# Performance work log

Hardware: AMD Instinct MI355X
Metric: run time of the kernel (lower is better)

The kernel has to match this reference:

```python
import jax, jax.numpy as jnp
import numpy as np

DIM = 64
HALF = DIM // 2
K = 8
B = 3.0
HID = 256
N = 65536
MIN_BW = 1e-3
MIN_BH = 1e-3
MIN_D = 1e-3


def _mlp(x, w0, b0, w1, b1, w2, b2):
    h = jnp.tanh(x @ w0 + b0)
    h = jnp.tanh(h @ w1 + b1)
    return h @ w2 + b2


def _unconstrained_rqs(x, uW, uH, uD, tail_bound):
    # x: [N, d]; uW, uH: [N, d, K]; uD: [N, d, K-1]
    # Faithful to Durkan/Karpathy unconstrained_RQS (forward, inverse=False).
    left, right, bottom, top = -tail_bound, tail_bound, -tail_bound, tail_bound
    inside = (x >= -tail_bound) & (x <= tail_bound)

    const = float(np.log(np.exp(1.0 - MIN_D) - 1.0))
    uD = jnp.pad(uD, ((0, 0), (0, 0), (1, 1)), constant_values=const)  # [N,d,K+1]

    widths = jax.nn.softmax(uW, axis=-1)
    widths = MIN_BW + (1.0 - MIN_BW * K) * widths
    cumw = jnp.cumsum(widths, axis=-1)
    cumw = jnp.pad(cumw, ((0, 0), (0, 0), (1, 0)))
    cumw = (right - left) * cumw + left
    cumw = cumw.at[..., 0].set(left).at[..., -1].set(right)
    widths = cumw[..., 1:] - cumw[..., :-1]

    derivs = MIN_D + jax.nn.softplus(uD)  # [N,d,K+1]

    heights = jax.nn.softmax(uH, axis=-1)
    heights = MIN_BH + (1.0 - MIN_BH * K) * heights
    cumh = jnp.cumsum(heights, axis=-1)
    cumh = jnp.pad(cumh, ((0, 0), (0, 0), (1, 0)))
    cumh = (top - bottom) * cumh + bottom
    cumh = cumh.at[..., 0].set(bottom).at[..., -1].set(top)
    heights = cumh[..., 1:] - cumh[..., :-1]

    # searchsorted: sum(x >= bin_locations) - 1, with eps on the last edge
    xin = jnp.clip(x, left, right)  # safe values for the outside-interval lanes
    locs = cumw.at[..., -1].add(1e-6)
    bin_idx = jnp.sum(xin[..., None] >= locs, axis=-1) - 1
    bin_idx = jnp.clip(bin_idx, 0, K - 1)

    def g(a):
        return jnp.take_along_axis(a, bin_idx[..., None], axis=-1)[..., 0]

    in_cumw = g(cumw)
    in_w = g(widths)
    in_cumh = g(cumh)
    in_h = g(heights)
    in_delta = g(heights / widths)
    in_d = g(derivs)
    in_d1 = g(derivs[..., 1:])

    theta = (xin - in_cumw) / in_w
    tt = theta * (1.0 - theta)
    numer = in_h * (in_delta * theta * theta + in_d * tt)
    denom = in_delta + (in_d + in_d1 - 2.0 * in_delta) * tt
    out = in_cumh + numer / denom
    dnum = in_delta * in_delta * (in_d1 * theta * theta + 2.0 * in_delta * tt + in_d * (1.0 - theta) ** 2)
    lad = jnp.log(dnum) - 2.0 * jnp.log(denom)

    out = jnp.where(inside, out, x)
    lad = jnp.where(inside, lad, 0.0)
    return out, lad


def _coupling_params(out):
    # out: [N, HALF, 3K-1] -> W, H (softmax * 2B), D (softplus)
    W = out[..., :K]
    H = out[..., K:2 * K]
    D = out[..., 2 * K:]
    W = 2.0 * B * jax.nn.softmax(W, axis=-1)
    H = 2.0 * B * jax.nn.softmax(H, axis=-1)
    D = jax.nn.softplus(D)
    return W, H, D


def setup_inputs() -> dict:
    key = jax.random.key(0)
    ks = jax.random.split(key, 7)
    s = 0.05
    inp = {"x": jax.random.normal(ks[0], (N, DIM), dtype=jnp.float32)}
    out_dim = (3 * K - 1) * HALF
    for i, name in enumerate(["f1", "f2"]):
        kk = jax.random.split(ks[1 + i], 3)
        inp[f"{name}_w0"] = s * jax.random.normal(kk[0], (HALF, HID), dtype=jnp.float32)
        inp[f"{name}_b0"] = jnp.zeros((HID,), dtype=jnp.float32)
        inp[f"{name}_w1"] = s * jax.random.normal(kk[1], (HID, HID), dtype=jnp.float32)
        inp[f"{name}_b1"] = jnp.zeros((HID,), dtype=jnp.float32)
        inp[f"{name}_w2"] = s * jax.random.normal(kk[2], (HID, out_dim), dtype=jnp.float32)
        inp[f"{name}_b2"] = jnp.zeros((out_dim,), dtype=jnp.float32)
    return inp


def reference(x, f1_w0, f1_b0, f1_w1, f1_b1, f1_w2, f1_b2,
              f2_w0, f2_b0, f2_w1, f2_b1, f2_w2, f2_b2):
    lower, upper = x[:, :HALF], x[:, HALF:]

    out = _mlp(lower, f1_w0, f1_b0, f1_w1, f1_b1, f1_w2, f1_b2).reshape(-1, HALF, 3 * K - 1)
    W, H, D = _coupling_params(out)
    upper, ld = _unconstrained_rqs(upper, W, H, D, B)
    log_det = jnp.sum(ld, axis=1)

    out = _mlp(upper, f2_w0, f2_b0, f2_w1, f2_b1, f2_w2, f2_b2).reshape(-1, HALF, 3 * K - 1)
    W, H, D = _coupling_params(out)
    lower, ld = _unconstrained_rqs(lower, W, H, D, B)
    log_det = log_det + jnp.sum(ld, axis=1)

    return jnp.concatenate([lower, upper], axis=1), log_det
```

## Files before the change

### kernel.cpp

```cpp
#include <hip/hip_runtime.h>

#define NHALF 32
#define NDIM  64
#define NHID  256
#define NPAR  736

typedef unsigned short u16;
typedef unsigned int   u32;
typedef __attribute__((ext_vector_type(8))) short short8;
typedef __attribute__((ext_vector_type(4))) float f32x4;

__device__ __forceinline__ float bf2f(u16 h){ return __uint_as_float(((u32)h) << 16); }
__device__ __forceinline__ u16 f2bf(float f){
  u32 u = __float_as_uint(f);
  u += 0x7FFFu + ((u >> 16) & 1u);
  return (u16)(u >> 16);
}
__device__ __forceinline__ float frcp(float x){ return __builtin_amdgcn_rcpf(x); }
__device__ __forceinline__ float tanh_fast(float x){
  x = fminf(15.f, fmaxf(-15.f, x));
  float e = __expf(2.f * x);
  return 1.f - 2.f * frcp(e + 1.f);
}

__device__ __forceinline__ void gload16(const u16* g, u16* l){
  __builtin_amdgcn_global_load_lds(
      (const __attribute__((address_space(1))) unsigned int*)(g),
      (__attribute__((address_space(3))) unsigned int*)(l), 16, 0, 0);
}

template<bool TANH>
__global__ __launch_bounds__(256, 4)
void mfma_gemm(const u16* __restrict__ A, const u16* __restrict__ Wt,
               const float* __restrict__ bias, u16* __restrict__ C,
               int K, int Jreal)
{
  __shared__ __align__(16) u16 sm[16384];
  const int t    = threadIdx.x;
  const int lane = t & 63, w = t >> 6;
  const int wr   = w >> 1, wc = w & 1;
  const int lm   = lane & 15, lk = lane >> 4;
  const int row0 = blockIdx.x * 128;
  const int jb   = blockIdx.y * 128;

  f32x4 acc[4][4];
  #pragma unroll
  for (int i = 0; i < 4; i++)
    #pragma unroll
    for (int j = 0; j < 4; j++) acc[i][j] = (f32x4){0.f, 0.f, 0.f, 0.f};

  const int nk = K >> 5;

  auto stage = [&](int buf, int ks){
    const int kk = ks << 5;
    u16* base = sm + buf * 8192;
    #pragma unroll
    for (int h = 0; h < 2; h++){
      int s = w + h * 4;
      gload16(A  + (size_t)(row0 + s * 16 + lm) * K + kk + lk * 8, base + s * 512);
      gload16(Wt + (size_t)(jb   + s * 16 + lm) * K + kk + lk * 8, base + 4096 + s * 512);
    }
  };

  auto compute = [&](int buf){
    const u16* base = sm + buf * 8192;
    short8 a[4], b[4];
    #pragma unroll
    for (int i = 0; i < 4; i++){
      a[i] = *(const short8*)(base + (wr * 4 + i) * 512 + lane * 8);
      b[i] = *(const short8*)(base + 4096 + (wc * 4 + i) * 512 + lane * 8);
    }
    #pragma unroll
    for (int i = 0; i < 4; i++)
      #pragma unroll
      for (int j = 0; j < 4; j++)
        acc[i][j] = __builtin_amdgcn_mfma_f32_16x16x32_bf16(a[i], b[j], acc[i][j], 0, 0, 0);
  };

  stage(0, 0);
  __syncthreads();
  for (int ks = 0; ks < nk; ++ks){
    if (ks + 1 < nk) stage((ks + 1) & 1, ks + 1);
    compute(ks & 1);
    __syncthreads();
  }

  const int rbase = row0 + wr * 64;
  const int cbase = jb + wc * 64;
  u16* ep = sm + w * 2432;
  float bs[4];
  #pragma unroll
  for (int j = 0; j < 4; j++){
    int col = cbase + j * 16 + lm;
    bs[j] = (col < Jreal) ? bias[col] : 0.f;
  }
  const int lr8 = lane >> 3, lc8 = lane & 7;
  #pragma unroll
  for (int h = 0; h < 2; h++){
    #pragma unroll
    for (int ii = 0; ii < 2; ii++){
      int i = h * 2 + ii;
      #pragma unroll
      for (int j = 0; j < 4; j++){
        #pragma unroll
        for (int r = 0; r < 4; r++){
          float v = acc[i][j][r] + bs[j];
          if (TANH) v = tanh_fast(v);
          ep[(ii * 16 + lk * 4 + r) * 76 + j * 16 + lm] = f2bf(v);
        }
      }
    }
    #pragma unroll
    for (int pass = 0; pass < 4; pass++){
      int lr = pass * 8 + lr8;
      uint4 v = *(const uint4*)(ep + lr * 76 + lc8 * 8);
      int col0 = cbase + lc8 * 8;
      if (col0 + 7 < Jreal)
        *(uint4*)(C + (size_t)(rbase + h * 32 + lr) * Jreal + col0) = v;
    }
  }
}

__global__ __launch_bounds__(256)
void xconv_k(const float* __restrict__ in, u16* __restrict__ out, int col0){
  int tid = blockIdx.x * 256 + threadIdx.x;
  int row = tid >> 3, c4 = (tid & 7) << 2;
  float4 v = *(const float4*)(in + (size_t)row * NDIM + col0 + c4);
  ushort4 o; o.x = f2bf(v.x); o.y = f2bf(v.y); o.z = f2bf(v.z); o.w = f2bf(v.w);
  *(ushort4*)(out + (size_t)row * NHALF + c4) = o;
}

__global__ __launch_bounds__(256)
void wconv3_k(const float* __restrict__ W0, const float* __restrict__ W1,
              const float* __restrict__ W2,
              u16* __restrict__ w0t, u16* __restrict__ w1t, u16* __restrict__ w2t){
  int tid = blockIdx.x * 256 + threadIdx.x;
  if (tid < 8192){
    int n = tid >> 5, k = tid & 31;
    w0t[tid] = f2bf(W0[(size_t)k * 256 + n]);
  } else if (tid < 73728){
    int id = tid - 8192; int n = id >> 8, k = id & 255;
    w1t[id] = f2bf(W1[(size_t)k * 256 + n]);
  } else if (tid < 270336){
    int id = tid - 73728; int n = id >> 8, k = id & 255;
    w2t[id] = (n < 736) ? f2bf(W2[(size_t)k * 736 + n]) : (u16)0;
  }
}

template<int PHASE>
__global__ __launch_bounds__(256)
void spline_k(const float* __restrict__ x,
              const u16* __restrict__ params,
              float* __restrict__ out,
              float* __restrict__ ldp,
              float* __restrict__ ldout,
              int xcol)
{
  __shared__ u16 pb[8 * NPAR];
  const int t = threadIdx.x;
  const int s0 = blockIdx.x * 8;

  {
    const uint4* src = (const uint4*)(params + (size_t)s0 * NPAR);
    uint4* dst = (uint4*)pb;
    dst[t]       = src[t];
    dst[256 + t] = src[256 + t];
    if (t < 224) dst[512 + t] = src[512 + t];
  }
  __syncthreads();

  const int si = t >> 5, d = t & 31;
  const int s = s0 + si;
  const u16* pp = pb + si * NPAR + d * 23;
  float p[23];
  #pragma unroll
  for (int e = 0; e < 23; e++) p[e] = bf2f(pp[e]);

  float W6[8], H6[8];
  {
    float m = p[0];
    #pragma unroll
    for (int i = 1; i < 8; i++) m = fmaxf(m, p[i]);
    float sm = 0.f;
    #pragma unroll
    for (int i = 0; i < 8; i++){ W6[i] = __expf(p[i] - m); sm += W6[i]; }
    float r = 6.f * frcp(sm);
    #pragma unroll
    for (int i = 0; i < 8; i++) W6[i] *= r;
  }
  {
    float m = p[8];
    #pragma unroll
    for (int i = 1; i < 8; i++) m = fmaxf(m, p[8 + i]);
    float sm = 0.f;
    #pragma unroll
    for (int i = 0; i < 8; i++){ H6[i] = __expf(p[8 + i] - m); sm += H6[i]; }
    float r = 6.f * frcp(sm);
    #pragma unroll
    for (int i = 0; i < 8; i++) H6[i] *= r;
  }

  float wd[8], cumw[9];
  {
    float sm = 0.f;
    #pragma unroll
    for (int i = 0; i < 8; i++){ wd[i] = __expf(W6[i]); sm += wd[i]; }
    float r = 0.992f * frcp(sm);
    #pragma unroll
    for (int i = 0; i < 8; i++) wd[i] = 0.001f + wd[i] * r;
  }
  cumw[0] = -3.f;
  { float run = 0.f;
    #pragma unroll
    for (int i = 0; i < 8; i++){ run += wd[i]; cumw[i + 1] = 6.f * run - 3.f; } }
  cumw[8] = 3.f;
  #pragma unroll
  for (int i = 0; i < 8; i++) wd[i] = cumw[i + 1] - cumw[i];

  float hg[8], cumh[9];
  {
    float sm = 0.f;
    #pragma unroll
    for (int i = 0; i < 8; i++){ hg[i] = __expf(H6[i]); sm += hg[i]; }
    float r = 0.992f * frcp(sm);
    #pragma unroll
    for (int i = 0; i < 8; i++) hg[i] = 0.001f + hg[i] * r;
  }
  cumh[0] = -3.f;
  { float run = 0.f;
    #pragma unroll
    for (int i = 0; i < 8; i++){ run += hg[i]; cumh[i + 1] = 6.f * run - 3.f; } }
  cumh[8] = 3.f;
  #pragma unroll
  for (int i = 0; i < 8; i++) hg[i] = cumh[i + 1] - cumh[i];

  float dv[9];
  dv[0] = 1.f; dv[8] = 1.f;
  #pragma unroll
  for (int j = 0; j < 7; j++){
    float xx  = p[16 + j];
    float z   = __expf(-fabsf(xx));
    float sel = (xx >= 0.f) ? z : 1.f;
    dv[j + 1] = 0.001f + fmaxf(xx, 0.f) + __logf(1.f + z + sel);
  }

  const float xv  = x[(size_t)s * NDIM + xcol + d];
  const float xin = fminf(3.f, fmaxf(-3.f, xv));

  int b = 0;
  #pragma unroll
  for (int j = 1; j < 8; j++) b += (xin >= cumw[j]) ? 1 : 0;

  float in_cw = 0.f, in_w = 0.f, in_ch = 0.f, in_h = 0.f, in_d = 0.f, in_d1 = 0.f;
  #pragma unroll
  for (int j = 0; j < 8; j++){
    if (j == b){ in_cw = cumw[j]; in_w = wd[j]; in_ch = cumh[j];
                 in_h = hg[j];  in_d = dv[j]; in_d1 = dv[j + 1]; }
  }

  float rw    = frcp(in_w);
  float th    = (xin - in_cw) * rw;
  float tt    = th * (1.f - th);
  float delta = in_h * rw;
  float numer = in_h * (delta * th * th + in_d * tt);
  float denom = delta + (in_d + in_d1 - 2.f * delta) * tt;
  float rden  = frcp(denom);
  float outv  = in_ch + numer * rden;
  float omt   = 1.f - th;
  float dnum  = delta * delta * (in_d1 * th * th + 2.f * delta * tt + in_d * omt * omt);
  float lad   = __logf(dnum * rden * rden);

  bool inside = (xv >= -3.f) && (xv <= 3.f);
  outv = inside ? outv : xv;
  lad  = inside ? lad  : 0.f;

  out[(size_t)s * NDIM + xcol + d] = outv;

  float v = lad;
  #pragma unroll
  for (int mm = 1; mm < 32; mm <<= 1) v += __shfl_xor(v, mm, 64);
  if (d == 0){
    if (PHASE == 0) ldp[s] = v;
    else            ldout[s] = ldp[s] + v;
  }
}

extern "C" void kernel_launch(void* const* d_in, const int* in_sizes, int n_in,
                              void* d_out, int out_size, void* d_ws, size_t ws_size,
                              hipStream_t stream)
{
  const float* x    = (const float*)d_in[0];
  const float* f1w0 = (const float*)d_in[1];
  const float* f1b0 = (const float*)d_in[2];
  const float* f1w1 = (const float*)d_in[3];
  const float* f1b1 = (const float*)d_in[4];
  const float* f1w2 = (const float*)d_in[5];
  const float* f1b2 = (const float*)d_in[6];
  const float* f2w0 = (const float*)d_in[7];
  const float* f2b0 = (const float*)d_in[8];
  const float* f2w1 = (const float*)d_in[9];
  const float* f2b1 = (const float*)d_in[10];
  const float* f2w2 = (const float*)d_in[11];
  const float* f2b2 = (const float*)d_in[12];

  const int N = in_sizes[0] / NDIM;
  float* out = (float*)d_out;
  float* ldout = out + (size_t)N * NDIM;

  u16* h1 = (u16*)d_ws;
  u16* h2 = h1 + (size_t)N * NHID;
  u16* pr = h2 + (size_t)N * NHID;
  float* ld1 = (float*)(pr + (size_t)N * NPAR);
  u16* wb  = (u16*)(ld1 + N);
  u16* w0t = wb;
  u16* w1t = w0t + 256 * 32;
  u16* w2t = w1t + 256 * 256;
  u16* xb  = pr;

  dim3 blk(256);
  dim3 g256(N / 128, 2);
  dim3 g736(N / 128, 6);
  dim3 gw(1056);
  dim3 gx(N * 8 / 256);
  dim3 gs(N / 8);

  wconv3_k<<<gw, blk, 0, stream>>>(f1w0, f1w1, f1w2, w0t, w1t, w2t);
  xconv_k<<<gx, blk, 0, stream>>>(x, xb, 0);
  mfma_gemm<true ><<<g256, blk, 0, stream>>>(xb, w0t, f1b0, h1, 32,  256);
  mfma_gemm<true ><<<g256, blk, 0, stream>>>(h1, w1t, f1b1, h2, 256, 256);
  mfma_gemm<false><<<g736, blk, 0, stream>>>(h2, w2t, f1b2, pr, 256, 736);
  spline_k<0><<<gs, blk, 0, stream>>>(x, pr, out, ld1, ldout, NHALF);

  wconv3_k<<<gw, blk, 0, stream>>>(f2w0, f2w1, f2w2, w0t, w1t, w2t);
  xconv_k<<<gx, blk, 0, stream>>>(out, xb, NHALF);
  mfma_gemm<true ><<<g256, blk, 0, stream>>>(xb, w0t, f2b0, h1, 32,  256);
  mfma_gemm<true ><<<g256, blk, 0, stream>>>(h1, w1t, f2b1, h2, 256, 256);
  mfma_gemm<false><<<g736, blk, 0, stream>>>(h2, w2t, f2b2, pr, 256, 736);
  spline_k<1><<<gs, blk, 0, stream>>>(x, pr, out, ld1, ldout, 0);
}
```

Measured before the change: 354.2 us.

## Fuse the three MLP GEMMs and input conversion into one kernel

Replaces the x-to-bf16 conversion kernel and the three separate tiled GEMM launches per coupling layer with one fused kernel per 128-row block. The hidden activations stay in a swizzled LDS buffer instead of round-tripping through global memory, and the weight fragments are read directly from global/L2 rather than staged through LDS. This removes the h1/h2 global traffic and four launches per layer. In exchange it costs high register pressure (32 accumulator fragments), lower occupancy, no load/compute pipelining, and unvectorized scalar bf16 stores to the parameter buffer.

```diff
diff --git a/kernel.cpp b/kernel.cpp
--- a/kernel.cpp
+++ b/kernel.cpp
@@ -23,111 +23,128 @@
   return 1.f - 2.f * frcp(e + 1.f);
 }
 
-__device__ __forceinline__ void gload16(const u16* g, u16* l){
-  __builtin_amdgcn_global_load_lds(
-      (const __attribute__((address_space(1))) unsigned int*)(g),
-      (__attribute__((address_space(3))) unsigned int*)(l), 16, 0, 0);
-}
-
-template<bool TANH>
-__global__ __launch_bounds__(256, 4)
-void mfma_gemm(const u16* __restrict__ A, const u16* __restrict__ Wt,
-               const float* __restrict__ bias, u16* __restrict__ C,
-               int K, int Jreal)
+__device__ __forceinline__ int hoff(int row, int col){
+  return row * 264 + (col ^ (((row >> 2) & 3) << 3));
+}
+
+template<int XCOL>
+__global__ __launch_bounds__(256, 2)
+void mlp_fused(const float* __restrict__ X,
+               const u16* __restrict__ w0t,
+               const u16* __restrict__ w1t,
+               const u16* __restrict__ w2t,
+               const float* __restrict__ b0, const float* __restrict__ b1,
+               const float* __restrict__ b2,
+               u16* __restrict__ pr)
 {
-  __shared__ __align__(16) u16 sm[16384];
-  const int t    = threadIdx.x;
-  const int lane = t & 63, w = t >> 6;
-  const int wr   = w >> 1, wc = w & 1;
-  const int lm   = lane & 15, lk = lane >> 4;
+  __shared__ __align__(16) u16 hb[128 * 264];
+  const int t = threadIdx.x, lane = t & 63, w = t >> 6;
+  const int lm = lane & 15, lk = lane >> 4;
   const int row0 = blockIdx.x * 128;
-  const int jb   = blockIdx.y * 128;
-
-  f32x4 acc[4][4];
-  #pragma unroll
-  for (int i = 0; i < 4; i++)
-    #pragma unroll
-    for (int j = 0; j < 4; j++) acc[i][j] = (f32x4){0.f, 0.f, 0.f, 0.f};
-
-  const int nk = K >> 5;
-
-  auto stage = [&](int buf, int ks){
-    const int kk = ks << 5;
-    u16* base = sm + buf * 8192;
-    #pragma unroll
-    for (int h = 0; h < 2; h++){
-      int s = w + h * 4;
-      gload16(A  + (size_t)(row0 + s * 16 + lm) * K + kk + lk * 8, base + s * 512);
-      gload16(Wt + (size_t)(jb   + s * 16 + lm) * K + kk + lk * 8, base + 4096 + s * 512);
-    }
-  };
-
-  auto compute = [&](int buf){
-    const u16* base = sm + buf * 8192;
-    short8 a[4], b[4];
-    #pragma unroll
-    for (int i = 0; i < 4; i++){
-      a[i] = *(const short8*)(base + (wr * 4 + i) * 512 + lane * 8);
-      b[i] = *(const short8*)(base + 4096 + (wc * 4 + i) * 512 + lane * 8);
-    }
-    #pragma unroll
-    for (int i = 0; i < 4; i++)
-      #pragma unroll
-      for (int j = 0; j < 4; j++)
-        acc[i][j] = __builtin_amdgcn_mfma_f32_16x16x32_bf16(a[i], b[j], acc[i][j], 0, 0, 0);
-  };
-
-  stage(0, 0);
+  const int cb = w * 64;
+
+  f32x4 acc[8][4];
+  const f32x4 zf = (f32x4){0.f, 0.f, 0.f, 0.f};
+
+  {
+    short8 a[8];
+    #pragma unroll
+    for (int mf = 0; mf < 8; mf++){
+      const float* xp = X + (size_t)(row0 + mf * 16 + lm) * NDIM + XCOL + lk * 8;
+      float4 v0 = *(const float4*)xp;
+      float4 v1 = *(const float4*)(xp + 4);
+      u16 tmp[8];
+      tmp[0] = f2bf(v0.x); tmp[1] = f2bf(v0.y); tmp[2] = f2bf(v0.z); tmp[3] = f2bf(v0.w);
+      tmp[4] = f2bf(v1.x); tmp[5] = f2bf(v1.y); tmp[6] = f2bf(v1.z); tmp[7] = f2bf(v1.w);
+      a[mf] = *(const short8*)tmp;
+    }
+    #pragma unroll
+    for (int nf = 0; nf < 4; nf++){
+      short8 b = *(const short8*)(w0t + (size_t)(cb + nf * 16 + lm) * 32 + lk * 8);
+      #pragma unroll
+      for (int mf = 0; mf < 8; mf++)
+        acc[mf][nf] = __builtin_amdgcn_mfma_f32_16x16x32_bf16(a[mf], b, zf, 0, 0, 0);
+    }
+    #pragma unroll
+    for (int nf = 0; nf < 4; nf++){
+      int col = cb + nf * 16 + lm;
+      float bs = b0[col];
+      #pragma unroll
+      for (int mf = 0; mf < 8; mf++)
+        #pragma unroll
+        for (int r = 0; r < 4; r++)
+          hb[hoff(mf * 16 + lk * 4 + r, col)] = f2bf(tanh_fast(acc[mf][nf][r] + bs));
+    }
+  }
   __syncthreads();
-  for (int ks = 0; ks < nk; ++ks){
-    if (ks + 1 < nk) stage((ks + 1) & 1, ks + 1);
-    compute(ks & 1);
-    __syncthreads();
-  }
-
-  const int rbase = row0 + wr * 64;
-  const int cbase = jb + wc * 64;
-  u16* ep = sm + w * 2432;
-  float bs[4];
-  #pragma unroll
-  for (int j = 0; j < 4; j++){
-    int col = cbase + j * 16 + lm;
-    bs[j] = (col < Jreal) ? bias[col] : 0.f;
-  }
-  const int lr8 = lane >> 3, lc8 = lane & 7;
-  #pragma unroll
-  for (int h = 0; h < 2; h++){
-    #pragma unroll
-    for (int ii = 0; ii < 2; ii++){
-      int i = h * 2 + ii;
-      #pragma unroll
-      for (int j = 0; j < 4; j++){
+
+  #pragma unroll
+  for (int mf = 0; mf < 8; mf++)
+    #pragma unroll
+    for (int nf = 0; nf < 4; nf++) acc[mf][nf] = zf;
+  for (int ks = 0; ks < 8; ks++){
+    short8 av[8], bv[4];
+    #pragma unroll
+    for (int mf = 0; mf < 8; mf++)
+      av[mf] = *(const short8*)(hb + hoff(mf * 16 + lm, ks * 32 + lk * 8));
+    #pragma unroll
+    for (int nf = 0; nf < 4; nf++)
+      bv[nf] = *(const short8*)(w1t + (size_t)(cb + nf * 16 + lm) * 256 + ks * 32 + lk * 8);
+    #pragma unroll
+    for (int mf = 0; mf < 8; mf++)
+      #pragma unroll
+      for (int nf = 0; nf < 4; nf++)
+        acc[mf][nf] = __builtin_amdgcn_mfma_f32_16x16x32_bf16(av[mf], bv[nf], acc[mf][nf], 0, 0, 0);
+  }
+  __syncthreads();
+  {
+    #pragma unroll
+    for (int nf = 0; nf < 4; nf++){
+      int col = cb + nf * 16 + lm;
+      float bs = b1[col];
+      #pragma unroll
+      for (int mf = 0; mf < 8; mf++)
         #pragma unroll
-        for (int r = 0; r < 4; r++){
-          float v = acc[i][j][r] + bs[j];
-          if (TANH) v = tanh_fast(v);
-          ep[(ii * 16 + lk * 4 + r) * 76 + j * 16 + lm] = f2bf(v);
-        }
+        for (int r = 0; r < 4; r++)
+          hb[hoff(mf * 16 + lk * 4 + r, col)] = f2bf(tanh_fast(acc[mf][nf][r] + bs));
+    }
+  }
+  __syncthreads();
+
+  #pragma unroll 1
+  for (int p = 0; p < 3; p++){
+    const int cb2 = p * 256 + w * 64;
+    #pragma unroll
+    for (int mf = 0; mf < 8; mf++)
+      #pragma unroll
+      for (int nf = 0; nf < 4; nf++) acc[mf][nf] = zf;
+    for (int ks = 0; ks < 8; ks++){
+      short8 av[8], bv[4];
+      #pragma unroll
+      for (int mf = 0; mf < 8; mf++)
+        av[mf] = *(const short8*)(hb + hoff(mf * 16 + lm, ks * 32 + lk * 8));
+      #pragma unroll
+      for (int nf = 0; nf < 4; nf++)
+        bv[nf] = *(const short8*)(w2t + (size_t)(cb2 + nf * 16 + lm) * 256 + ks * 32 + lk * 8);
+      #pragma unroll
+      for (int mf = 0; mf < 8; mf++)
+        #pragma unroll
+        for (int nf = 0; nf < 4; nf++)
+          acc[mf][nf] = __builtin_amdgcn_mfma_f32_16x16x32_bf16(av[mf], bv[nf], acc[mf][nf], 0, 0, 0);
+    }
+    #pragma unroll
+    for (int nf = 0; nf < 4; nf++){
+      int col = cb2 + nf * 16 + lm;
+      if (col < NPAR){
+        float bs = b2[col];
+        #pragma unroll
+        for (int mf = 0; mf < 8; mf++)
+          #pragma unroll
+          for (int r = 0; r < 4; r++)
+            pr[(size_t)(row0 + mf * 16 + lk * 4 + r) * NPAR + col] = f2bf(acc[mf][nf][r] + bs);
       }
     }
-    #pragma unroll
-    for (int pass = 0; pass < 4; pass++){
-      int lr = pass * 8 + lr8;
-      uint4 v = *(const uint4*)(ep + lr * 76 + lc8 * 8);
-      int col0 = cbase + lc8 * 8;
-      if (col0 + 7 < Jreal)
-        *(uint4*)(C + (size_t)(rbase + h * 32 + lr) * Jreal + col0) = v;
-    }
-  }
-}
-
-__global__ __launch_bounds__(256)
-void xconv_k(const float* __restrict__ in, u16* __restrict__ out, int col0){
-  int tid = blockIdx.x * 256 + threadIdx.x;
-  int row = tid >> 3, c4 = (tid & 7) << 2;
-  float4 v = *(const float4*)(in + (size_t)row * NDIM + col0 + c4);
-  ushort4 o; o.x = f2bf(v.x); o.y = f2bf(v.y); o.z = f2bf(v.z); o.w = f2bf(v.w);
-  *(ushort4*)(out + (size_t)row * NHALF + c4) = o;
+  }
 }
 
 __global__ __launch_bounds__(256)
@@ -307,34 +324,22 @@
   float* out = (float*)d_out;
   float* ldout = out + (size_t)N * NDIM;
 
-  u16* h1 = (u16*)d_ws;
-  u16* h2 = h1 + (size_t)N * NHID;
-  u16* pr = h2 + (size_t)N * NHID;
+  u16* pr = (u16*)d_ws;
   float* ld1 = (float*)(pr + (size_t)N * NPAR);
-  u16* wb  = (u16*)(ld1 + N);
-  u16* w0t = wb;
+  u16* w0t = (u16*)(ld1 + N);
   u16* w1t = w0t + 256 * 32;
   u16* w2t = w1t + 256 * 256;
-  u16* xb  = pr;
 
   dim3 blk(256);
-  dim3 g256(N / 128, 2);
-  dim3 g736(N / 128, 6);
+  dim3 gm(N / 128);
   dim3 gw(1056);
-  dim3 gx(N * 8 / 256);
   dim3 gs(N / 8);
 
   wconv3_k<<<gw, blk, 0, stream>>>(f1w0, f1w1, f1w2, w0t, w1t, w2t);
-  xconv_k<<<gx, blk, 0, stream>>>(x, xb, 0);
-  mfma_gemm<true ><<<g256, blk, 0, stream>>>(xb, w0t, f1b0, h1, 32,  256);
-  mfma_gemm<true ><<<g256, blk, 0, stream>>>(h1, w1t, f1b1, h2, 256, 256);
-  mfma_gemm<false><<<g736, blk, 0, stream>>>(h2, w2t, f1b2, pr, 256, 736);
+  mlp_fused<0><<<gm, blk, 0, stream>>>(x, w0t, w1t, w2t, f1b0, f1b1, f1b2, pr);
   spline_k<0><<<gs, blk, 0, stream>>>(x, pr, out, ld1, ldout, NHALF);
 
   wconv3_k<<<gw, blk, 0, stream>>>(f2w0, f2w1, f2w2, w0t, w1t, w2t);
-  xconv_k<<<gx, blk, 0, stream>>>(out, xb, NHALF);
-  mfma_gemm<true ><<<g256, blk, 0, stream>>>(xb, w0t, f2b0, h1, 32,  256);
-  mfma_gemm<true ><<<g256, blk, 0, stream>>>(h1, w1t, f2b1, h2, 256, 256);
-  mfma_gemm<false><<<g736, blk, 0, stream>>>(h2, w2t, f2b2, pr, 256, 736);
+  mlp_fused<NHALF><<<gm, blk, 0, stream>>>(out, w0t, w1t, w2t, f2b0, f2b1, f2b2, pr);
   spline_k<1><<<gs, blk, 0, stream>>>(x, pr, out, ld1, ldout, 0);
 }
```

Measured after the change: 287.4 us. 1.23x faster.
